# Kernel tuning notes

Measured on AMD Instinct MI355X. Metric: run time of the kernel, lower is better.

## Reference

```python
import jax, jax.numpy as jnp
import numpy as np

EPS_STD = 1e-5   # PNA std aggregator epsilon
EPS_GN = 1e-5    # GraphNorm epsilon


def setup_inputs() -> dict:
    key = jax.random.key(0)
    B, N, C = 8, 256, 128
    ks = jax.random.split(key, 8)
    w = lambda k, sh: jax.random.normal(k, sh, jnp.float32) * 0.05
    return {
        "x": jax.random.normal(ks[0], (B, N, C), jnp.float32),
        "edge": jax.random.normal(ks[1], (B, N * N, C), jnp.float32),
        "W_edge": w(ks[2], (C, C)), "b_edge": jnp.zeros((C,), jnp.float32),
        "W_pre": w(ks[3], (3 * C, C)), "b_pre": jnp.zeros((C,), jnp.float32),
        "W_post": w(ks[4], (5 * C, C)), "b_post": jnp.zeros((C,), jnp.float32),
        "W_lin": w(ks[5], (C, C)), "b_lin": jnp.zeros((C,), jnp.float32),
        "gn_weight": jnp.ones((C,), jnp.float32),
        "gn_bias": jnp.zeros((C,), jnp.float32),
        "gn_alpha": jnp.ones((C,), jnp.float32),
    }


def reference(x, edge, W_edge, b_edge, W_pre, b_pre, W_post, b_post,
              W_lin, b_lin, gn_weight, gn_bias, gn_alpha):
    B, N, C = x.shape
    res = x
    # edge e = i*N + j: source j -> target i  => reshape to [B, i(target), j(source), C]
    e = edge.reshape(B, N, N, C)
    e_enc = e @ W_edge + b_edge                               # edge_encoder
    x_i = jnp.broadcast_to(x[:, :, None, :], (B, N, N, C))    # target feats
    x_j = jnp.broadcast_to(x[:, None, :, :], (B, N, N, C))    # source feats
    h = jnp.concatenate([x_i, x_j, e_enc], axis=-1)           # [B,N,N,3C]
    m = h @ W_pre + b_pre                                     # pre-MLP messages [B,N,N,C]
    # PNA aggregators over source axis j (graph is fully connected, degree == N)
    mean = m.mean(axis=2)
    mn = m.min(axis=2)
    mx = m.max(axis=2)
    var = (m * m).mean(axis=2) - mean * mean
    std = jnp.sqrt(jax.nn.relu(var) + EPS_STD)
    agg = jnp.concatenate([mean, mn, mx, std], axis=-1)       # [B,N,4C]
    out = jnp.concatenate([x, agg], axis=-1) @ W_post + b_post  # post-MLP [B,N,C]
    out = out @ W_lin + b_lin                                  # final linear
    # GraphNorm with batch=None in the original: stats over ALL B*N nodes
    flat = out.reshape(B * N, C)
    mu = flat.mean(axis=0, keepdims=True)
    centered = flat - gn_alpha * mu
    v = (centered * centered).mean(axis=0, keepdims=True)
    normed = gn_weight * centered / jnp.sqrt(v + EPS_GN) + gn_bias
    y = jax.nn.relu(normed).reshape(B, N, C)
    return y + res
```

## Files before the change

kernel.cpp:

```cpp
#include <hip/hip_runtime.h>
#include <hip/hip_bf16.h>
#include <stdint.h>

typedef __attribute__((ext_vector_type(8))) short bf16x8;
typedef __attribute__((ext_vector_type(4))) float f32x4;
typedef __attribute__((ext_vector_type(4))) unsigned int u32x4;

#define NB 256
#define CC 128

static __device__ __forceinline__ unsigned int cvt_pk_bf16(float lo, float hi) {
  unsigned int r;
  asm("v_cvt_pk_bf16_f32 %0, %1, %2" : "=v"(r) : "v"(lo), "v"(hi));
  return r;
}
static __device__ __forceinline__ uint16_t f2bf(float f) {
  unsigned u = __builtin_bit_cast(unsigned, f);
  return (uint16_t)((u + 0x7FFFu + ((u >> 16) & 1u)) >> 16);
}

__global__ void k_prep(const float* __restrict__ W_edge, const float* __restrict__ b_edge,
                       const float* __restrict__ W_pre, const float* __restrict__ b_pre,
                       const float* __restrict__ x,
                       uint16_t* __restrict__ wct, float* __restrict__ bc2,
                       float* __restrict__ At, unsigned* __restrict__ bvl) {
  const int c = threadIdx.x;
  if (blockIdx.x < 128) {
    const int k = blockIdx.x;
    float acc = 0.f;
    for (int q = 0; q < CC; ++q)
      acc += W_edge[k * CC + q] * W_pre[(2 * CC + q) * CC + c];
    wct[c * CC + k] = f2bf(acc);
    if (k == 0) {
      float a2 = b_pre[c];
      for (int q = 0; q < CC; ++q) a2 += b_edge[q] * W_pre[(2 * CC + q) * CC + c];
      bc2[c] = a2;
    }
  } else {
    const int m0 = (blockIdx.x - 128) * 2;
    __shared__ float xs[2][CC];
    xs[0][c] = x[(size_t)m0 * CC + c];
    xs[1][c] = x[(size_t)(m0 + 1) * CC + c];
    __syncthreads();
    float a0 = 0.f, a1 = 0.f, v0 = 0.f, v1 = 0.f;
#pragma unroll 4
    for (int k = 0; k < CC; ++k) {
      const float w1 = W_pre[k * CC + c];
      const float w2 = W_pre[(CC + k) * CC + c];
      a0 += xs[0][k] * w1; a1 += xs[1][k] * w1;
      v0 += xs[0][k] * w2; v1 += xs[1][k] * w2;
    }
    At[(size_t)m0 * CC + c] = a0;       At[(size_t)(m0 + 1) * CC + c] = a1;
    const float p0 = __shfl_down(v0, 16);
    const float p1 = __shfl_down(v1, 16);
    if ((c & 31) < 16) {
      const int di = (c >> 5) * 16 + (c & 15);
      bvl[(size_t)m0 * 64 + di]       = ((unsigned)f2bf(p0) << 16) | f2bf(v0);
      bvl[(size_t)(m0 + 1) * 64 + di] = ((unsigned)f2bf(p1) << 16) | f2bf(v1);
    }
  }
}

__global__ __launch_bounds__(256, 4) void k_edge(
    const float* __restrict__ edge, const uint16_t* __restrict__ wct,
    const unsigned* __restrict__ bvl, const float* __restrict__ At,
    const float* __restrict__ bc2, float* __restrict__ agg) {
  __shared__ __align__(16) char ebuf[2][16 * 272];
  __shared__ __align__(16) char bvbuf[2][16 * 272];

  const int blk  = blockIdx.x;
  const int b    = blk >> 8;
  const int tid  = threadIdx.x;
  const int lane = tid & 63;
  const int wv   = tid >> 6;
  const int g    = lane >> 4;
  const int lr   = lane & 15;
  const int cb   = wv * 32;

  bf16x8 bfr[2][4];
#pragma unroll
  for (int t = 0; t < 2; ++t) {
    const uint16_t* p1 = wct + (cb + t * 16 + lr) * CC + g * 8;
#pragma unroll
    for (int ks = 0; ks < 4; ++ks)
      bfr[t][ks] = *(const bf16x8*)(p1 + ks * 32);
  }
  asm volatile("s_waitcnt vmcnt(0)" ::: "memory");

  const char* egbase  = (const char*)(edge + (size_t)blk * (NB * CC));
  const char* bvgbase = (const char*)(bvl + (size_t)b * (NB * 64));
  const int sdst = (tid >> 4) * 272 + (tid & 15) * 16;

  f32x4 eA0, eA1, eB0, eB1;
  u32x4 vA, vB;

  auto LOADA = [&](int t) {
    const f32x4* s = (const f32x4*)(egbase + (size_t)t * 8192 + tid * 32);
    eA0 = s[0]; eA1 = s[1];
    vA = *(const u32x4*)(bvgbase + (size_t)t * 4096 + tid * 16);
  };
  auto LOADB = [&](int t) {
    const f32x4* s = (const f32x4*)(egbase + (size_t)t * 8192 + tid * 32);
    eB0 = s[0]; eB1 = s[1];
    vB = *(const u32x4*)(bvgbase + (size_t)t * 4096 + tid * 16);
  };
  auto STORE = [&](char* eb_, char* bb_, const f32x4& e0, const f32x4& e1, const u32x4& v) {
    u32x4 w;
    w.x = cvt_pk_bf16(e0.x, e0.y); w.y = cvt_pk_bf16(e0.z, e0.w);
    w.z = cvt_pk_bf16(e1.x, e1.y); w.w = cvt_pk_bf16(e1.z, e1.w);
    *(u32x4*)(eb_ + sdst) = w;
    *(u32x4*)(bb_ + sdst) = v;
  };

  float sum0 = 0.f, sum1 = 0.f, ssq0 = 0.f, ssq1 = 0.f;
  float mn0 = 1e30f, mn1 = 1e30f, mx0 = -1e30f, mx1 = -1e30f;

  auto COMPUTE = [&](const char* eb_, const char* bb_) {
    const char* eb = eb_ + lr * 272;
    f32x4 acc0 = {0.f, 0.f, 0.f, 0.f}, acc1 = {0.f, 0.f, 0.f, 0.f};
#pragma unroll
    for (int ks = 0; ks < 4; ++ks) {
      bf16x8 af = *(const bf16x8*)(eb + g * 16 + ks * 64);
      acc0 = __builtin_amdgcn_mfma_f32_16x16x32_bf16(af, bfr[0][ks], acc0, 0, 0, 0);
      acc1 = __builtin_amdgcn_mfma_f32_16x16x32_bf16(af, bfr[1][ks], acc1, 0, 0, 0);
    }
#pragma unroll
    for (int r = 0; r < 4; ++r) {
      const int row = g * 4 + r;
      const unsigned pv = *(const unsigned*)(bb_ + row * 272 + wv * 64 + lr * 4);
      const float bv0 = __builtin_bit_cast(float, pv << 16);
      const float bv1 = __builtin_bit_cast(float, pv & 0xffff0000u);
      float s0 = acc0[r] + bv0;
      float s1 = acc1[r] + bv1;
      sum0 += s0; ssq0 = fmaf(s0, s0, ssq0);
      mn0 = fminf(mn0, s0); mx0 = fmaxf(mx0, s0);
      sum1 += s1; ssq1 = fmaf(s1, s1, ssq1);
      mn1 = fminf(mn1, s1); mx1 = fmaxf(mx1, s1);
    }
  };

  LOADA(0); LOADB(1);
  __builtin_amdgcn_sched_barrier(0);

#pragma unroll 1
  for (int tt = 0; tt < 16; tt += 2) {
    __builtin_amdgcn_s_barrier();
    asm volatile("s_waitcnt vmcnt(3)" ::: "memory");
    __builtin_amdgcn_sched_barrier(0);
    STORE(ebuf[0], bvbuf[0], eA0, eA1, vA);
    asm volatile("s_waitcnt lgkmcnt(0)" ::: "memory");
    __builtin_amdgcn_sched_barrier(0);
    __builtin_amdgcn_s_barrier();
    if (tt + 2 < 16) LOADA(tt + 2);
    __builtin_amdgcn_sched_barrier(0);
    COMPUTE(ebuf[0], bvbuf[0]);
    __builtin_amdgcn_s_barrier();
    if (tt < 14) { asm volatile("s_waitcnt vmcnt(3)" ::: "memory"); }
    else         { asm volatile("s_waitcnt vmcnt(0)" ::: "memory"); }
    __builtin_amdgcn_sched_barrier(0);
    STORE(ebuf[1], bvbuf[1], eB0, eB1, vB);
    asm volatile("s_waitcnt lgkmcnt(0)" ::: "memory");
    __builtin_amdgcn_sched_barrier(0);
    __builtin_amdgcn_s_barrier();
    if (tt + 3 < 16) LOADB(tt + 3);
    __builtin_amdgcn_sched_barrier(0);
    COMPUTE(ebuf[1], bvbuf[1]);
  }

#pragma unroll
  for (int m = 16; m <= 32; m <<= 1) {
    sum0 += __shfl_xor(sum0, m); ssq0 += __shfl_xor(ssq0, m);
    mn0 = fminf(mn0, __shfl_xor(mn0, m)); mx0 = fmaxf(mx0, __shfl_xor(mx0, m));
    sum1 += __shfl_xor(sum1, m); ssq1 += __shfl_xor(ssq1, m);
    mn1 = fminf(mn1, __shfl_xor(mn1, m)); mx1 = fmaxf(mx1, __shfl_xor(mx1, m));
  }
  if (g == 0) {
#pragma unroll
    for (int t = 0; t < 2; ++t) {
      const int col = cb + t * 16 + lr;
      const float s   = t ? sum1 : sum0;
      const float q   = t ? ssq1 : ssq0;
      const float mnv = t ? mn1 : mn0;
      const float mxv = t ? mx1 : mx0;
      const float tt2 = At[blk * CC + col] + bc2[col];
      const float mean = s * (1.f / NB);
      const float var = q * (1.f / NB) - mean * mean;
      const float sd = sqrtf(fmaxf(var, 0.f) + 1e-5f);
      float* ap = agg + (size_t)blk * (4 * CC) + col;
      ap[0]      = tt2 + mean;
      ap[CC]     = tt2 + mnv;
      ap[2 * CC] = tt2 + mxv;
      ap[3 * CC] = sd;
    }
  }
}

__global__ __launch_bounds__(256) void k_post(
    const float* __restrict__ x, const float* __restrict__ agg,
    const float* __restrict__ W_post, const float* __restrict__ b_post,
    const float* __restrict__ W_lin, const float* __restrict__ b_lin,
    float* __restrict__ outl, float* __restrict__ psum, float* __restrict__ psq) {
  __shared__ float hx[4][5 * CC];
  __shared__ float o1[4][CC];
  __shared__ float pl[4][CC];
  const int blk = blockIdx.x;
  const int t = threadIdx.x;
  const int row0 = blk * 4;

  for (int idx = t; idx < 4 * 5 * CC; idx += 256) {
    int r = idx / (5 * CC), col = idx - r * (5 * CC);
    hx[r][col] = (col < CC) ? x[(size_t)(row0 + r) * CC + col]
                            : agg[(size_t)(row0 + r) * (4 * CC) + (col - CC)];
  }
  __syncthreads();

  const int c = t & (CC - 1);
  const int rh = t >> 7;
  float acc[2] = {b_post[c], b_post[c]};
  for (int k = 0; k < 5 * CC; k += 4) {
    float w0 = W_post[(k + 0) * CC + c];
    float w1 = W_post[(k + 1) * CC + c];
    float w2 = W_post[(k + 2) * CC + c];
    float w3 = W_post[(k + 3) * CC + c];
#pragma unroll
    for (int i = 0; i < 2; ++i) {
      const f32x4 h4 = *(const f32x4*)&hx[2 * i + rh][k];
      acc[i] += h4.x * w0 + h4.y * w1 + h4.z * w2 + h4.w * w3;
    }
  }
#pragma unroll
  for (int i = 0; i < 2; ++i) o1[2 * i + rh][c] = acc[i];
  __syncthreads();

  float a2[2] = {b_lin[c], b_lin[c]};
  for (int k = 0; k < CC; k += 4) {
    float w0 = W_lin[(k + 0) * CC + c];
    float w1 = W_lin[(k + 1) * CC + c];
    float w2 = W_lin[(k + 2) * CC + c];
    float w3 = W_lin[(k + 3) * CC + c];
#pragma unroll
    for (int i = 0; i < 2; ++i) {
      const f32x4 h4 = *(const f32x4*)&o1[2 * i + rh][k];
      a2[i] += h4.x * w0 + h4.y * w1 + h4.z * w2 + h4.w * w3;
    }
  }
  float ps = 0.f, pq = 0.f;
#pragma unroll
  for (int i = 0; i < 2; ++i) {
    outl[(size_t)(row0 + 2 * i + rh) * CC + c] = a2[i];
    ps += a2[i]; pq += a2[i] * a2[i];
  }
  pl[rh][c] = ps; pl[2 + rh][c] = pq;
  __syncthreads();
  if (t < CC) {
    psum[blk * CC + t] = pl[0][t] + pl[1][t];
    psq[blk * CC + t]  = pl[2][t] + pl[3][t];
  }
}

__global__ __launch_bounds__(256) void k_apply(
    const float* __restrict__ psum, const float* __restrict__ psq,
    const float* __restrict__ outl, const float* __restrict__ x,
    const float* __restrict__ gw, const float* __restrict__ gb,
    const float* __restrict__ alpha, float* __restrict__ y) {
  __shared__ float red[4][CC];
  __shared__ float smu[CC], siv[CC];
  const int t = threadIdx.x;
  const int c = t & (CC - 1);
  const int h = t >> 7;
  float s = 0.f, q = 0.f;
#pragma unroll 4
  for (int i = 0; i < 256; ++i) {
    const int r = h * 256 + i;
    s += psum[r * CC + c];
    q += psq[r * CC + c];
  }
  red[h][c] = s; red[2 + h][c] = q;
  __syncthreads();
  if (t < CC) {
    const float ss = red[0][t] + red[1][t];
    const float qq = red[2][t] + red[3][t];
    const float mu = ss * (1.f / 2048.f);
    const float ex2 = qq * (1.f / 2048.f);
    const float amu = alpha[t] * mu;
    const float v = ex2 - 2.f * amu * mu + amu * amu;
    smu[t] = amu;
    siv[t] = gw[t] / sqrtf(v + 1e-5f);
  }
  __syncthreads();
  const int row0 = blockIdx.x * 8;
#pragma unroll
  for (int r = 0; r < 8; r += 2) {
    const int idx = (row0 + r + h) * CC + c;
    const float o = outl[idx];
    const float val = (o - smu[c]) * siv[c] + gb[c];
    y[idx] = fmaxf(val, 0.f) + x[idx];
  }
}

extern "C" void kernel_launch(void* const* d_in, const int* in_sizes, int n_in,
                              void* d_out, int out_size, void* d_ws, size_t ws_size,
                              hipStream_t stream) {
  const float* x      = (const float*)d_in[0];
  const float* edge   = (const float*)d_in[1];
  const float* W_edge = (const float*)d_in[2];
  const float* b_edge = (const float*)d_in[3];
  const float* W_pre  = (const float*)d_in[4];
  const float* b_pre  = (const float*)d_in[5];
  const float* W_post = (const float*)d_in[6];
  const float* b_post = (const float*)d_in[7];
  const float* W_lin  = (const float*)d_in[8];
  const float* b_lin  = (const float*)d_in[9];
  const float* gw     = (const float*)d_in[10];
  const float* gb     = (const float*)d_in[11];
  const float* alpha  = (const float*)d_in[12];
  float* y = (float*)d_out;

  float* wsf = (float*)d_ws;
  float* bc2   = wsf;
  float* At    = wsf + 128;
  float* agg   = wsf + 262272;
  float* outl  = wsf + 1310848;
  float* psum  = wsf + 1572992;
  float* psq   = wsf + 1638528;
  uint16_t* wct = (uint16_t*)(wsf + 1704064);
  unsigned* bvl = (unsigned*)(wsf + 1712256);

  k_prep<<<1152, 128, 0, stream>>>(W_edge, b_edge, W_pre, b_pre, x, wct, bc2, At, bvl);
  k_edge<<<2048, 256, 0, stream>>>(edge, wct, bvl, At, bc2, agg);
  k_post<<<512, 256, 0, stream>>>(x, agg, W_post, b_post, W_lin, b_lin, outl, psum, psq);
  k_apply<<<256, 256, 0, stream>>>(psum, psq, outl, x, gw, gb, alpha, y);
}
```

Measured before the change: 106.7 us.

## Load edge tiles directly into MFMA register fragments, dropping LDS staging

Result: slower. 186.9 us (+75.2%).

```diff
diff --git a/kernel.cpp b/kernel.cpp
--- a/kernel.cpp
+++ b/kernel.cpp
@@ -61,13 +61,10 @@
   }
 }
 
-__global__ __launch_bounds__(256, 4) void k_edge(
+__global__ __launch_bounds__(256, 3) void k_edge(
     const float* __restrict__ edge, const uint16_t* __restrict__ wct,
     const unsigned* __restrict__ bvl, const float* __restrict__ At,
     const float* __restrict__ bc2, float* __restrict__ agg) {
-  __shared__ __align__(16) char ebuf[2][16 * 272];
-  __shared__ __align__(16) char bvbuf[2][16 * 272];
-
   const int blk  = blockIdx.x;
   const int b    = blk >> 8;
   const int tid  = threadIdx.x;
@@ -87,51 +84,66 @@
   }
   asm volatile("s_waitcnt vmcnt(0)" ::: "memory");
 
-  const char* egbase  = (const char*)(edge + (size_t)blk * (NB * CC));
-  const char* bvgbase = (const char*)(bvl + (size_t)b * (NB * 64));
-  const int sdst = (tid >> 4) * 272 + (tid & 15) * 16;
-
-  f32x4 eA0, eA1, eB0, eB1;
-  u32x4 vA, vB;
+  const char* eg0 = (const char*)(edge + (size_t)blk * (NB * CC)) + lr * 512 + g * 32;
+  const char* bg0 = (const char*)(bvl + (size_t)b * (NB * 64)) + g * 4 * 256 + wv * 64 + lr * 4;
+
+  f32x4 eA[8], eB[8];
+  unsigned bvA[4], bvB[4];
 
   auto LOADA = [&](int t) {
-    const f32x4* s = (const f32x4*)(egbase + (size_t)t * 8192 + tid * 32);
-    eA0 = s[0]; eA1 = s[1];
-    vA = *(const u32x4*)(bvgbase + (size_t)t * 4096 + tid * 16);
+#pragma unroll
+    for (int ks = 0; ks < 4; ++ks) {
+      eA[ks]     = *(const f32x4*)(eg0 + (size_t)t * 8192 + ks * 128);
+      eA[ks + 4] = *(const f32x4*)(eg0 + (size_t)t * 8192 + ks * 128 + 16);
+    }
+#pragma unroll
+    for (int r = 0; r < 4; ++r)
+      bvA[r] = *(const unsigned*)(bg0 + (size_t)t * 4096 + r * 256);
   };
   auto LOADB = [&](int t) {
-    const f32x4* s = (const f32x4*)(egbase + (size_t)t * 8192 + tid * 32);
-    eB0 = s[0]; eB1 = s[1];
-    vB = *(const u32x4*)(bvgbase + (size_t)t * 4096 + tid * 16);
-  };
-  auto STORE = [&](char* eb_, char* bb_, const f32x4& e0, const f32x4& e1, const u32x4& v) {
-    u32x4 w;
-    w.x = cvt_pk_bf16(e0.x, e0.y); w.y = cvt_pk_bf16(e0.z, e0.w);
-    w.z = cvt_pk_bf16(e1.x, e1.y); w.w = cvt_pk_bf16(e1.z, e1.w);
-    *(u32x4*)(eb_ + sdst) = w;
-    *(u32x4*)(bb_ + sdst) = v;
+#pragma unroll
+    for (int ks = 0; ks < 4; ++ks) {
+      eB[ks]     = *(const f32x4*)(eg0 + (size_t)t * 8192 + ks * 128);
+      eB[ks + 4] = *(const f32x4*)(eg0 + (size_t)t * 8192 + ks * 128 + 16);
+    }
+#pragma unroll
+    for (int r = 0; r < 4; ++r)
+      bvB[r] = *(const unsigned*)(bg0 + (size_t)t * 4096 + r * 256);
   };
 
   float sum0 = 0.f, sum1 = 0.f, ssq0 = 0.f, ssq1 = 0.f;
   float mn0 = 1e30f, mn1 = 1e30f, mx0 = -1e30f, mx1 = -1e30f;
 
-  auto COMPUTE = [&](const char* eb_, const char* bb_) {
-    const char* eb = eb_ + lr * 272;
+  bf16x8 af[4];
+  float bvf[8];
+
+  auto CVT = [&](const f32x4* E, const unsigned* BV) {
+#pragma unroll
+    for (int ks = 0; ks < 4; ++ks) {
+      u32x4 aw;
+      aw.x = cvt_pk_bf16(E[ks].x, E[ks].y);
+      aw.y = cvt_pk_bf16(E[ks].z, E[ks].w);
+      aw.z = cvt_pk_bf16(E[ks + 4].x, E[ks + 4].y);
+      aw.w = cvt_pk_bf16(E[ks + 4].z, E[ks + 4].w);
+      af[ks] = __builtin_bit_cast(bf16x8, aw);
+    }
+#pragma unroll
+    for (int r = 0; r < 4; ++r) {
+      bvf[r]     = __builtin_bit_cast(float, BV[r] << 16);
+      bvf[4 + r] = __builtin_bit_cast(float, BV[r] & 0xffff0000u);
+    }
+  };
+  auto MAC = [&]() {
     f32x4 acc0 = {0.f, 0.f, 0.f, 0.f}, acc1 = {0.f, 0.f, 0.f, 0.f};
 #pragma unroll
     for (int ks = 0; ks < 4; ++ks) {
-      bf16x8 af = *(const bf16x8*)(eb + g * 16 + ks * 64);
-      acc0 = __builtin_amdgcn_mfma_f32_16x16x32_bf16(af, bfr[0][ks], acc0, 0, 0, 0);
-      acc1 = __builtin_amdgcn_mfma_f32_16x16x32_bf16(af, bfr[1][ks], acc1, 0, 0, 0);
+      acc0 = __builtin_amdgcn_mfma_f32_16x16x32_bf16(af[ks], bfr[0][ks], acc0, 0, 0, 0);
+      acc1 = __builtin_amdgcn_mfma_f32_16x16x32_bf16(af[ks], bfr[1][ks], acc1, 0, 0, 0);
     }
 #pragma unroll
     for (int r = 0; r < 4; ++r) {
-      const int row = g * 4 + r;
-      const unsigned pv = *(const unsigned*)(bb_ + row * 272 + wv * 64 + lr * 4);
-      const float bv0 = __builtin_bit_cast(float, pv << 16);
-      const float bv1 = __builtin_bit_cast(float, pv & 0xffff0000u);
-      float s0 = acc0[r] + bv0;
-      float s1 = acc1[r] + bv1;
+      float s0 = acc0[r] + bvf[r];
+      float s1 = acc1[r] + bvf[4 + r];
       sum0 += s0; ssq0 = fmaf(s0, s0, ssq0);
       mn0 = fminf(mn0, s0); mx0 = fmaxf(mx0, s0);
       sum1 += s1; ssq1 = fmaf(s1, s1, ssq1);
@@ -144,27 +156,21 @@
 
 #pragma unroll 1
   for (int tt = 0; tt < 16; tt += 2) {
-    __builtin_amdgcn_s_barrier();
-    asm volatile("s_waitcnt vmcnt(3)" ::: "memory");
-    __builtin_amdgcn_sched_barrier(0);
-    STORE(ebuf[0], bvbuf[0], eA0, eA1, vA);
-    asm volatile("s_waitcnt lgkmcnt(0)" ::: "memory");
-    __builtin_amdgcn_sched_barrier(0);
-    __builtin_amdgcn_s_barrier();
+    asm volatile("s_waitcnt vmcnt(12)" ::: "memory");
+    __builtin_amdgcn_sched_barrier(0);
+    CVT(eA, bvA);
+    __builtin_amdgcn_sched_barrier(0);
     if (tt + 2 < 16) LOADA(tt + 2);
     __builtin_amdgcn_sched_barrier(0);
-    COMPUTE(ebuf[0], bvbuf[0]);
-    __builtin_amdgcn_s_barrier();
-    if (tt < 14) { asm volatile("s_waitcnt vmcnt(3)" ::: "memory"); }
+    MAC();
+    if (tt < 14) { asm volatile("s_waitcnt vmcnt(12)" ::: "memory"); }
     else         { asm volatile("s_waitcnt vmcnt(0)" ::: "memory"); }
     __builtin_amdgcn_sched_barrier(0);
-    STORE(ebuf[1], bvbuf[1], eB0, eB1, vB);
-    asm volatile("s_waitcnt lgkmcnt(0)" ::: "memory");
-    __builtin_amdgcn_sched_barrier(0);
-    __builtin_amdgcn_s_barrier();
+    CVT(eB, bvB);
+    __builtin_amdgcn_sched_barrier(0);
     if (tt + 3 < 16) LOADB(tt + 3);
     __builtin_amdgcn_sched_barrier(0);
-    COMPUTE(ebuf[1], bvbuf[1]);
+    MAC();
   }
 
 #pragma unroll
```

## Split edge aggregation over source-node quarters with a separate combine kernel

Applied to the files above, without the earlier changes.

After: 128.9 us. +20.9%, slower.

```diff
diff --git a/kernel.cpp b/kernel.cpp
--- a/kernel.cpp
+++ b/kernel.cpp
@@ -63,19 +63,23 @@
 
 __global__ __launch_bounds__(256, 4) void k_edge(
     const float* __restrict__ edge, const uint16_t* __restrict__ wct,
-    const unsigned* __restrict__ bvl, const float* __restrict__ At,
-    const float* __restrict__ bc2, float* __restrict__ agg) {
+    const unsigned* __restrict__ bvl,
+    float* __restrict__ pS, float* __restrict__ pQ,
+    float* __restrict__ pMn, float* __restrict__ pMx) {
   __shared__ __align__(16) char ebuf[2][16 * 272];
   __shared__ __align__(16) char bvbuf[2][16 * 272];
 
   const int blk  = blockIdx.x;
-  const int b    = blk >> 8;
+  const int iblk = blk >> 2;
+  const int jq   = blk & 3;
+  const int b    = iblk >> 8;
   const int tid  = threadIdx.x;
   const int lane = tid & 63;
   const int wv   = tid >> 6;
   const int g    = lane >> 4;
   const int lr   = lane & 15;
   const int cb   = wv * 32;
+  const int t0   = jq * 4;
 
   bf16x8 bfr[2][4];
 #pragma unroll
@@ -87,7 +91,7 @@
   }
   asm volatile("s_waitcnt vmcnt(0)" ::: "memory");
 
-  const char* egbase  = (const char*)(edge + (size_t)blk * (NB * CC));
+  const char* egbase  = (const char*)(edge + (size_t)iblk * (NB * CC));
   const char* bvgbase = (const char*)(bvl + (size_t)b * (NB * 64));
   const int sdst = (tid >> 4) * 272 + (tid & 15) * 16;
 
@@ -139,11 +143,11 @@
     }
   };
 
-  LOADA(0); LOADB(1);
+  LOADA(t0); LOADB(t0 + 1);
   __builtin_amdgcn_sched_barrier(0);
 
 #pragma unroll 1
-  for (int tt = 0; tt < 16; tt += 2) {
+  for (int tt = 0; tt < 4; tt += 2) {
     __builtin_amdgcn_s_barrier();
     asm volatile("s_waitcnt vmcnt(3)" ::: "memory");
     __builtin_amdgcn_sched_barrier(0);
@@ -151,18 +155,18 @@
     asm volatile("s_waitcnt lgkmcnt(0)" ::: "memory");
     __builtin_amdgcn_sched_barrier(0);
     __builtin_amdgcn_s_barrier();
-    if (tt + 2 < 16) LOADA(tt + 2);
+    if (tt + 2 < 4) LOADA(t0 + tt + 2);
     __builtin_amdgcn_sched_barrier(0);
     COMPUTE(ebuf[0], bvbuf[0]);
     __builtin_amdgcn_s_barrier();
-    if (tt < 14) { asm volatile("s_waitcnt vmcnt(3)" ::: "memory"); }
-    else         { asm volatile("s_waitcnt vmcnt(0)" ::: "memory"); }
+    if (tt < 2) { asm volatile("s_waitcnt vmcnt(3)" ::: "memory"); }
+    else        { asm volatile("s_waitcnt vmcnt(0)" ::: "memory"); }
     __builtin_amdgcn_sched_barrier(0);
     STORE(ebuf[1], bvbuf[1], eB0, eB1, vB);
     asm volatile("s_waitcnt lgkmcnt(0)" ::: "memory");
     __builtin_amdgcn_sched_barrier(0);
     __builtin_amdgcn_s_barrier();
-    if (tt + 3 < 16) LOADB(tt + 3);
+    if (tt + 3 < 4) LOADB(t0 + tt + 3);
     __builtin_amdgcn_sched_barrier(0);
     COMPUTE(ebuf[1], bvbuf[1]);
   }
@@ -178,21 +182,38 @@
 #pragma unroll
     for (int t = 0; t < 2; ++t) {
       const int col = cb + t * 16 + lr;
-      const float s   = t ? sum1 : sum0;
-      const float q   = t ? ssq1 : ssq0;
-      const float mnv = t ? mn1 : mn0;
-      const float mxv = t ? mx1 : mx0;
-      const float tt2 = At[blk * CC + col] + bc2[col];
-      const float mean = s * (1.f / NB);
-      const float var = q * (1.f / NB) - mean * mean;
-      const float sd = sqrtf(fmaxf(var, 0.f) + 1e-5f);
-      float* ap = agg + (size_t)blk * (4 * CC) + col;
-      ap[0]      = tt2 + mean;
-      ap[CC]     = tt2 + mnv;
-      ap[2 * CC] = tt2 + mxv;
-      ap[3 * CC] = sd;
-    }
-  }
+      const size_t o = (size_t)blk * CC + col;
+      pS[o]  = t ? sum1 : sum0;
+      pQ[o]  = t ? ssq1 : ssq0;
+      pMn[o] = t ? mn1 : mn0;
+      pMx[o] = t ? mx1 : mx0;
+    }
+  }
+}
+
+__global__ __launch_bounds__(128) void k_comb(
+    const float* __restrict__ pS, const float* __restrict__ pQ,
+    const float* __restrict__ pMn, const float* __restrict__ pMx,
+    const float* __restrict__ At, const float* __restrict__ bc2,
+    float* __restrict__ agg) {
+  const int i = blockIdx.x;
+  const int c = threadIdx.x;
+  float s = 0.f, q = 0.f, mn = 1e30f, mx = -1e30f;
+#pragma unroll
+  for (int jq = 0; jq < 4; ++jq) {
+    const size_t o = ((size_t)i * 4 + jq) * CC + c;
+    s += pS[o]; q += pQ[o];
+    mn = fminf(mn, pMn[o]); mx = fmaxf(mx, pMx[o]);
+  }
+  const float tt = At[(size_t)i * CC + c] + bc2[c];
+  const float mean = s * (1.f / NB);
+  const float var = q * (1.f / NB) - mean * mean;
+  const float sd = sqrtf(fmaxf(var, 0.f) + 1e-5f);
+  float* ap = agg + (size_t)i * (4 * CC) + c;
+  ap[0]      = tt + mean;
+  ap[CC]     = tt + mn;
+  ap[2 * CC] = tt + mx;
+  ap[3 * CC] = sd;
 }
 
 __global__ __launch_bounds__(256) void k_post(
@@ -325,9 +346,14 @@
   float* psq   = wsf + 1638528;
   uint16_t* wct = (uint16_t*)(wsf + 1704064);
   unsigned* bvl = (unsigned*)(wsf + 1712256);
+  float* pS  = wsf + 1843328;
+  float* pQ  = wsf + 2891904;
+  float* pMn = wsf + 3940480;
+  float* pMx = wsf + 4989056;
 
   k_prep<<<1152, 128, 0, stream>>>(W_edge, b_edge, W_pre, b_pre, x, wct, bc2, At, bvl);
-  k_edge<<<2048, 256, 0, stream>>>(edge, wct, bvl, At, bc2, agg);
+  k_edge<<<8192, 256, 0, stream>>>(edge, wct, bvl, pS, pQ, pMn, pMx);
+  k_comb<<<2048, 128, 0, stream>>>(pS, pQ, pMn, pMx, At, bc2, agg);
   k_post<<<512, 256, 0, stream>>>(x, agg, W_post, b_post, W_lin, b_lin, outl, psum, psq);
   k_apply<<<256, 256, 0, stream>>>(psum, psq, outl, x, gw, gb, alpha, y);
 }
```
